# Performance work log

Hardware: AMD Instinct MI355X
Metric: run time of the kernel (lower is better)

Reference implementation:

```python
import math
import jax, jax.numpy as jnp
import numpy as np

EMBED = 512
HEADS = 8
EPS = 1e-5


def _ln(x, gamma, beta):
    mu = jnp.mean(x, axis=-1, keepdims=True)
    var = jnp.mean(jnp.square(x - mu), axis=-1, keepdims=True)
    return (x - mu) * jax.lax.rsqrt(var + EPS) * gamma + beta


def setup_inputs() -> dict:
    key = jax.random.key(0)
    ks = jax.random.split(key, 16)
    D = EMBED
    s = 0.02
    inp = {
        "moves_embeddings": jax.random.normal(ks[0], (4, 2048, D), dtype=jnp.float32),
        "wq": jax.random.normal(ks[1], (D, D), dtype=jnp.float32) * s,
        "bq": jnp.zeros((D,), jnp.float32),
        "wk": jax.random.normal(ks[2], (D, D), dtype=jnp.float32) * s,
        "bk": jnp.zeros((D,), jnp.float32),
        "wv": jax.random.normal(ks[3], (D, D), dtype=jnp.float32) * s,
        "bv": jnp.zeros((D,), jnp.float32),
        "wo": jax.random.normal(ks[4], (D, D), dtype=jnp.float32) * s,
        "bo": jnp.zeros((D,), jnp.float32),
        "w_up": jax.random.normal(ks[5], (D, 4 * D), dtype=jnp.float32) * s,
        "b_up": jnp.zeros((4 * D,), jnp.float32),
        "w_down": jax.random.normal(ks[6], (4 * D, D), dtype=jnp.float32) * s,
        "b_down": jnp.zeros((D,), jnp.float32),
        "g1": jnp.ones((D,), jnp.float32),
        "beta1": jnp.zeros((D,), jnp.float32),
        "g2": jnp.ones((D,), jnp.float32),
        "beta2": jnp.zeros((D,), jnp.float32),
    }
    return inp


def reference(moves_embeddings, wq, bq, wk, bk, wv, bv, wo, bo,
              w_up, b_up, w_down, b_down, g1, beta1, g2, beta2):
    x = moves_embeddings  # [B, S, D]
    B, S, D = x.shape
    Hd = D // HEADS
    # QKV projections, split heads -> [B, H, S, Hd]
    q = (x @ wq + bq).reshape(B, S, HEADS, Hd).transpose(0, 2, 1, 3)
    k = (x @ wk + bk).reshape(B, S, HEADS, Hd).transpose(0, 2, 1, 3)
    v = (x @ wv + bv).reshape(B, S, HEADS, Hd).transpose(0, 2, 1, 3)
    # NOTE: original scales by sqrt(embedding_dim), not sqrt(head_dim)
    scores = jnp.einsum('bhqd,bhkd->bhqk', q, k) / math.sqrt(D)
    attn = jax.nn.softmax(scores, axis=-1)
    ctx = jnp.einsum('bhqk,bhkd->bhqd', attn, v)
    ctx = ctx.transpose(0, 2, 1, 3).reshape(B, S, D)
    y = ctx @ wo + bo
    x = _ln(x + y, g1, beta1)
    # FFN with exact (erf) GELU, matching torch nn.GELU default
    h = jax.nn.gelu(x @ w_up + b_up, approximate=False)
    y = h @ w_down + b_down
    return _ln(x + y, g2, beta2)
```

## Files before the change

### kernel.cpp

```cpp
#include <hip/hip_runtime.h>
#include <math.h>

#define D 512
#define NHEADS 8
#define HD 64
#define SEQ 2048
#define BATCH 4
#define MROWS (BATCH*SEQ)
#define QKVSTR 1536
#define ATT_QSCALE 0.06376228841159383f

typedef short bf16x8 __attribute__((ext_vector_type(8)));
typedef float f32x4 __attribute__((ext_vector_type(4)));
typedef float f32x16 __attribute__((ext_vector_type(16)));

__device__ __forceinline__ ushort f2bf(float f) {
    union { float f; unsigned u; } v; v.f = f;
    unsigned r = (v.u + 0x7fffu + ((v.u >> 16) & 1u)) >> 16;
    return (ushort)r;
}
__device__ __forceinline__ float bf2f(ushort u) {
    union { unsigned u; float f; } v; v.u = ((unsigned)u) << 16; return v.f;
}

__device__ __forceinline__ unsigned cvt_pk_bf16(float lo, float hi_) {
    unsigned r;
    asm("v_cvt_pk_bf16_f32 %0, %1, %2" : "=v"(r) : "v"(lo), "v"(hi_));
    return r;
}

__device__ __forceinline__ float exp2_hw(float x) {
    float r;
    asm("v_exp_f32 %0, %1" : "=v"(r) : "v"(x));
    return r;
}

__device__ __forceinline__ void plswap(unsigned &a, unsigned &b) {
    asm("v_permlane32_swap_b32 %0, %1" : "+v"(a), "+v"(b));
}
__device__ __forceinline__ void plswapf(float &a, float &b) {
    union { float f; unsigned u; } ua, ub;
    ua.f = a; ub.f = b;
    asm("v_permlane32_swap_b32 %0, %1" : "+v"(ua.u), "+v"(ub.u));
    a = ua.f; b = ub.f;
}

__device__ __forceinline__ void gload16(const void* g, void* lds) {
    __builtin_amdgcn_global_load_lds(
        (const __attribute__((address_space(1))) unsigned int*)(uintptr_t)g,
        (__attribute__((address_space(3))) unsigned int*)(uintptr_t)lds,
        16, 0, 0);
}

template<int GELU, int OBF16, int SPLITK>
__global__ __launch_bounds__(512)
void gemm_mfma8(const ushort* __restrict__ A, const ushort* __restrict__ Bt,
                const float* __restrict__ bias, void* __restrict__ Cp,
                void* __restrict__ Cp2, int M, int N, int K)
{
    __shared__ ushort As[2][128 * 64];
    __shared__ ushort Bs[2][128 * 64];

    const int tid = threadIdx.x;
    const int w = tid >> 6, lane = tid & 63;
    const int lr = lane & 15, lg = lane >> 4;
    const int wr = w >> 2, wc = w & 3;
    const int row0 = blockIdx.y * 128, col0 = blockIdx.x * 128;
    const int kLen = SPLITK ? (K >> 1) : K;
    const int kOff = SPLITK ? blockIdx.z * kLen : 0;

    const int srow = lane >> 3;
    const int schunk = (lane & 7) ^ srow;

    const ushort* aSrc = A  + (size_t)(row0 + w * 16 + srow) * K + kOff + schunk * 8;
    const ushort* bSrc = Bt + (size_t)(col0 + w * 16 + srow) * K + kOff + schunk * 8;

    f32x4 acc[4][2] = {};

    auto STAGE = [&](int buf, int k0) {
        ushort* aD = &As[buf][(w * 16) * 64];
        ushort* bD = &Bs[buf][(w * 16) * 64];
        gload16(aSrc + k0,                 aD);
        gload16(aSrc + (size_t)8 * K + k0, aD + 8 * 64);
        gload16(bSrc + k0,                 bD);
        gload16(bSrc + (size_t)8 * K + k0, bD + 8 * 64);
    };

    auto COMPUTE = [&](int buf) {
        const ushort* AsB = As[buf];
        const ushort* BsB = Bs[buf];
        #pragma unroll
        for (int kc = 0; kc < 2; ++kc) {
            bf16x8 af[4], bfr[2];
            #pragma unroll
            for (int mt = 0; mt < 4; ++mt)
                af[mt] = *(const bf16x8*)&AsB[(wr * 64 + mt * 16 + lr) * 64 +
                                             (((kc * 4 + lg) ^ (lr & 7)) * 8)];
            #pragma unroll
            for (int nt = 0; nt < 2; ++nt)
                bfr[nt] = *(const bf16x8*)&BsB[(wc * 32 + nt * 16 + lr) * 64 +
                                              (((kc * 4 + lg) ^ (lr & 7)) * 8)];
            __builtin_amdgcn_s_setprio(1);
            #pragma unroll
            for (int mt = 0; mt < 4; ++mt)
                #pragma unroll
                for (int nt = 0; nt < 2; ++nt)
                    acc[mt][nt] = __builtin_amdgcn_mfma_f32_16x16x32_bf16(
                        af[mt], bfr[nt], acc[mt][nt], 0, 0, 0);
            __builtin_amdgcn_s_setprio(0);
        }
    };

    const int nk = kLen >> 6;
    STAGE(0, 0);
    __syncthreads();
    for (int t = 0; t < nk; ++t) {
        if (t + 1 < nk) STAGE((t + 1) & 1, (t + 1) << 6);
        COMPUTE(t & 1);
        __syncthreads();
    }

    float* Pp = SPLITK ? (blockIdx.z ? (float*)Cp2 : (float*)Cp) : (float*)Cp;
    #pragma unroll
    for (int nt = 0; nt < 2; ++nt) {
        const int col = col0 + wc * 32 + nt * 16 + lr;
        const float bv = SPLITK ? 0.f : bias[col];
        #pragma unroll
        for (int mt = 0; mt < 4; ++mt) {
            #pragma unroll
            for (int i = 0; i < 4; ++i) {
                float o = acc[mt][nt][i] + bv;
                if (GELU) o = 0.5f * o * (1.0f + erff(o * 0.70710678118654752f));
                const size_t idx = (size_t)(row0 + wr * 64 + mt * 16 + lg * 4 + i) * N + col;
                if (OBF16) ((ushort*)Cp)[idx] = f2bf(o);
                else       Pp[idx] = o;
            }
        }
    }
}

__global__ __launch_bounds__(512)
void gemm_qkv8(const ushort* __restrict__ A, const ushort* __restrict__ Bt,
               const float* __restrict__ bias, ushort* __restrict__ qkv,
               ushort* __restrict__ vt)
{
    __shared__ ushort As[2][128 * 64];
    __shared__ ushort Bs[2][128 * 64];

    const int tid = threadIdx.x;
    const int w = tid >> 6, lane = tid & 63;
    const int lr = lane & 15, lg = lane >> 4;
    const int wr = w >> 2, wc = w & 3;
    const int row0 = blockIdx.y * 128, col0 = blockIdx.x * 128;
    const int K = 512;

    const int srow = lane >> 3;
    const int schunk = (lane & 7) ^ srow;

    const ushort* aSrc = A  + (size_t)(row0 + w * 16 + srow) * K + schunk * 8;
    const ushort* bSrc = Bt + (size_t)(col0 + w * 16 + srow) * K + schunk * 8;

    f32x4 acc[4][2] = {};

    auto STAGE = [&](int buf, int k0) {
        ushort* aD = &As[buf][(w * 16) * 64];
        ushort* bD = &Bs[buf][(w * 16) * 64];
        gload16(aSrc + k0,                 aD);
        gload16(aSrc + (size_t)8 * K + k0, aD + 8 * 64);
        gload16(bSrc + k0,                 bD);
        gload16(bSrc + (size_t)8 * K + k0, bD + 8 * 64);
    };

    auto COMPUTE = [&](int buf) {
        const ushort* AsB = As[buf];
        const ushort* BsB = Bs[buf];
        #pragma unroll
        for (int kc = 0; kc < 2; ++kc) {
            bf16x8 af[4], bfr[2];
            #pragma unroll
            for (int mt = 0; mt < 4; ++mt)
                af[mt] = *(const bf16x8*)&AsB[(wr * 64 + mt * 16 + lr) * 64 +
                                             (((kc * 4 + lg) ^ (lr & 7)) * 8)];
            #pragma unroll
            for (int nt = 0; nt < 2; ++nt)
                bfr[nt] = *(const bf16x8*)&BsB[(wc * 32 + nt * 16 + lr) * 64 +
                                              (((kc * 4 + lg) ^ (lr & 7)) * 8)];
            __builtin_amdgcn_s_setprio(1);
            #pragma unroll
            for (int mt = 0; mt < 4; ++mt)
                #pragma unroll
                for (int nt = 0; nt < 2; ++nt)
                    acc[mt][nt] = __builtin_amdgcn_mfma_f32_16x16x32_bf16(
                        af[mt], bfr[nt], acc[mt][nt], 0, 0, 0);
            __builtin_amdgcn_s_setprio(0);
        }
    };

    STAGE(0, 0);
    __syncthreads();
    for (int t = 0; t < 8; ++t) {
        if (t + 1 < 8) STAGE((t + 1) & 1, (t + 1) << 6);
        COMPUTE(t & 1);
        __syncthreads();
    }

    #pragma unroll
    for (int nt = 0; nt < 2; ++nt) {
        const int col = col0 + wc * 32 + nt * 16 + lr;
        const float bv = bias[col];
        if (col < 1024) {
            const float sc = (col < 512) ? ATT_QSCALE : 1.0f;
            #pragma unroll
            for (int mt = 0; mt < 4; ++mt) {
                #pragma unroll
                for (int i = 0; i < 4; ++i) {
                    const float o = (acc[mt][nt][i] + bv) * sc;
                    qkv[(size_t)(row0 + wr * 64 + mt * 16 + lg * 4 + i) * QKVSTR + col] = f2bf(o);
                }
            }
        } else {
            const int hh = (col - 1024) >> 6, d = (col - 1024) & 63;
            #pragma unroll
            for (int mt = 0; mt < 4; ++mt) {
                const int rowb = row0 + wr * 64 + mt * 16 + lg * 4;
                const int bb = rowb >> 11, ss = rowb & (SEQ - 1);
                ushort4 o4;
                o4.x = f2bf(acc[mt][nt][0] + bv);
                o4.y = f2bf(acc[mt][nt][1] + bv);
                o4.z = f2bf(acc[mt][nt][2] + bv);
                o4.w = f2bf(acc[mt][nt][3] + bv);
                *(ushort4*)&vt[((size_t)(bb * NHEADS + hh) * HD + d) * SEQ + ss] = o4;
            }
        }
    }
}

#define KBLK 64
#define NKT (1024 / KBLK)

__global__ __launch_bounds__(512, 4)
void attn_mfma(const ushort* __restrict__ qkv, const ushort* __restrict__ vt,
               ushort* __restrict__ ctx)
{
    __shared__ __align__(16) ushort smem[2][2][2][64 * 64];

    const int tid = threadIdx.x;
    const int lane = tid & 63;
    const int l32 = lane & 31, hi = lane >> 5;
    const int w = tid >> 6;
    const int qsub = w & 3, half = w >> 2;
    const int qt = blockIdx.x, h = blockIdx.y, b = blockIdx.z;
    const int q0 = qt * 128 + qsub * 32;
    const int kbase = half * 1024;

    const size_t seqbase = (size_t)b * SEQ;
    const ushort* Qp = qkv + (seqbase + q0 + l32) * QKVSTR + h * HD;
    const ushort* Kg = qkv + seqbase * QKVSTR + 512 + h * HD;
    const ushort* Vg = vt + (size_t)(b * NHEADS + h) * HD * SEQ;

    bf16x8 qf[4];
    #pragma unroll
    for (int c = 0; c < 4; ++c) qf[c] = *(const bf16x8*)&Qp[c * 16 + hi * 8];

    const int srow = lane >> 3;
    const int sslot = (lane & 7) ^ srow;
    const ushort* pK = Kg + (size_t)(kbase + qsub * 16 + srow) * QKVSTR + sslot * 8;
    const ushort* pV = Vg + (size_t)(qsub * 16 + srow) * SEQ + kbase + sslot * 8;

    f32x16 o0 = {}, o1 = {};
    float l = 0.f;

    auto STAGE = [&](int buf) {
        ushort* dK = &smem[buf][half][0][(qsub * 16) * 64];
        ushort* dV = &smem[buf][half][1][(qsub * 16) * 64];
        gload16(pK,                      dK);
        gload16(pK + (size_t)8 * QKVSTR, dK + 8 * 64);
        gload16(pV,                      dV);
        gload16(pV + (size_t)8 * SEQ,    dV + 8 * 64);
        pK += (size_t)KBLK * QKVSTR;
        pV += KBLK;
    };

    auto COMPUTE = [&](int buf) {
        const ushort* KsH = &smem[buf][half][0][0];
        const ushort* VsH = &smem[buf][half][1][0];

        f32x16 s0 = {}, s1 = {};
        __builtin_amdgcn_s_setprio(1);
        #pragma unroll
        for (int c = 0; c < 4; ++c) {
            const bf16x8 kf0 = *(const bf16x8*)&KsH[l32 * 64 + (((2 * c + hi) ^ (l32 & 7)) * 8)];
            s0 = __builtin_amdgcn_mfma_f32_32x32x16_bf16(kf0, qf[c], s0, 0, 0, 0);
        }
        #pragma unroll
        for (int c = 0; c < 4; ++c) {
            const bf16x8 kf1 = *(const bf16x8*)&KsH[(32 + l32) * 64 + (((2 * c + hi) ^ (l32 & 7)) * 8)];
            s1 = __builtin_amdgcn_mfma_f32_32x32x16_bf16(kf1, qf[c], s1, 0, 0, 0);
        }
        __builtin_amdgcn_s_setprio(0);

        float ts = 0.f;
        #pragma unroll
        for (int r = 0; r < 16; ++r) {
            s0[r] = exp2_hw(s0[r]); ts += s0[r];
            s1[r] = exp2_hw(s1[r]); ts += s1[r];
        }
        l += ts;

        unsigned wp[16];
        #pragma unroll
        for (int j = 0; j < 8; ++j) wp[j]     = cvt_pk_bf16(s0[2 * j], s0[2 * j + 1]);
        #pragma unroll
        for (int j = 0; j < 8; ++j) wp[8 + j] = cvt_pk_bf16(s1[2 * j], s1[2 * j + 1]);
        plswap(wp[0], wp[2]);  plswap(wp[1], wp[3]);
        plswap(wp[4], wp[6]);  plswap(wp[5], wp[7]);
        plswap(wp[8], wp[10]); plswap(wp[9], wp[11]);
        plswap(wp[12], wp[14]); plswap(wp[13], wp[15]);
        union { unsigned u[4]; bf16x8 v; } pb[4];
        #pragma unroll
        for (int kg = 0; kg < 4; ++kg) {
            pb[kg].u[0] = wp[kg * 4 + 0];
            pb[kg].u[1] = wp[kg * 4 + 1];
            pb[kg].u[2] = wp[kg * 4 + 2];
            pb[kg].u[3] = wp[kg * 4 + 3];
        }

        __builtin_amdgcn_s_setprio(1);
        #pragma unroll
        for (int kg = 0; kg < 4; ++kg) {
            const bf16x8 vf0 = *(const bf16x8*)&VsH[l32 * 64 + (((2 * kg + hi) ^ (l32 & 7)) * 8)];
            o0 = __builtin_amdgcn_mfma_f32_32x32x16_bf16(vf0, pb[kg].v, o0, 0, 0, 0);
        }
        #pragma unroll
        for (int kg = 0; kg < 4; ++kg) {
            const bf16x8 vf1 = *(const bf16x8*)&VsH[(32 + l32) * 64 + (((2 * kg + hi) ^ (l32 & 7)) * 8)];
            o1 = __builtin_amdgcn_mfma_f32_32x32x16_bf16(vf1, pb[kg].v, o1, 0, 0, 0);
        }
        __builtin_amdgcn_s_setprio(0);
    };

    STAGE(0);
    __syncthreads();
    for (int tt = 0; tt < NKT; tt += 2) {
        if (tt + 1 < NKT) STAGE(1);
        COMPUTE(0);
        __syncthreads();
        if (tt + 2 < NKT) STAGE(0);
        COMPUTE(1);
        __syncthreads();
    }

    { float a_ = l, b_ = l; plswapf(a_, b_); l = a_ + b_; }

    float* so = (float*)smem;
    float* sl = (float*)((char*)smem + 4 * 64 * 33 * 4);
    if (half) {
        float* row = so + (qsub * 64 + lane) * 33;
        #pragma unroll
        for (int r = 0; r < 16; ++r) row[r] = o0[r];
        #pragma unroll
        for (int r = 0; r < 16; ++r) row[16 + r] = o1[r];
        sl[qsub * 64 + lane] = l;
    }
    __syncthreads();
    if (!half) {
        const float lb = sl[qsub * 64 + lane];
        const float* row = so + (qsub * 64 + lane) * 33;
        const float inv = 1.f / (l + lb);

        ushort* dst = ctx + (seqbase + q0 + l32) * D + h * HD;
        #pragma unroll
        for (int g = 0; g < 4; ++g) {
            ushort4 t0, t1;
            t0.x = f2bf((o0[g * 4 + 0] + row[g * 4 + 0]) * inv);
            t0.y = f2bf((o0[g * 4 + 1] + row[g * 4 + 1]) * inv);
            t0.z = f2bf((o0[g * 4 + 2] + row[g * 4 + 2]) * inv);
            t0.w = f2bf((o0[g * 4 + 3] + row[g * 4 + 3]) * inv);
            t1.x = f2bf((o1[g * 4 + 0] + row[16 + g * 4 + 0]) * inv);
            t1.y = f2bf((o1[g * 4 + 1] + row[16 + g * 4 + 1]) * inv);
            t1.z = f2bf((o1[g * 4 + 2] + row[16 + g * 4 + 2]) * inv);
            t1.w = f2bf((o1[g * 4 + 3] + row[16 + g * 4 + 3]) * inv);
            *(ushort4*)&dst[g * 8 + hi * 4]      = t0;
            *(ushort4*)&dst[32 + g * 8 + hi * 4] = t1;
        }
    }
}

template<int RESBF, int OUTBF>
__global__ __launch_bounds__(256)
void add_ln3(const void* __restrict__ res, const float* __restrict__ b0,
             const float* __restrict__ b1, const float* __restrict__ bias,
             const float* __restrict__ g, const float* __restrict__ beta,
             float* __restrict__ outf, ushort* __restrict__ outb)
{
    const int wave = threadIdx.x >> 6, lane = threadIdx.x & 63;
    const size_t row = (size_t)blockIdx.x * 4 + wave;

    float xr[8];
    if (RESBF) {
        const ushort* pr = (const ushort*)res + row * D + lane * 8;
        const ushort4 r0 = *(const ushort4*)pr;
        const ushort4 r1 = *(const ushort4*)(pr + 4);
        xr[0] = bf2f(r0.x); xr[1] = bf2f(r0.y); xr[2] = bf2f(r0.z); xr[3] = bf2f(r0.w);
        xr[4] = bf2f(r1.x); xr[5] = bf2f(r1.y); xr[6] = bf2f(r1.z); xr[7] = bf2f(r1.w);
    } else {
        const float* pr = (const float*)res + row * D + lane * 8;
        const float4 r0 = *(const float4*)pr;
        const float4 r1 = *(const float4*)(pr + 4);
        xr[0] = r0.x; xr[1] = r0.y; xr[2] = r0.z; xr[3] = r0.w;
        xr[4] = r1.x; xr[5] = r1.y; xr[6] = r1.z; xr[7] = r1.w;
    }

    const float* p0 = &b0[row * D + lane * 8];
    const float* p1 = &b1[row * D + lane * 8];
    const float4 c0 = *(const float4*)p0;
    const float4 c1 = *(const float4*)(p0 + 4);
    const float4 d0 = *(const float4*)p1;
    const float4 d1 = *(const float4*)(p1 + 4);
    const float4 bb0 = *(const float4*)&bias[lane * 8];
    const float4 bb1 = *(const float4*)&bias[lane * 8 + 4];

    float x[8];
    x[0] = xr[0] + c0.x + d0.x + bb0.x; x[1] = xr[1] + c0.y + d0.y + bb0.y;
    x[2] = xr[2] + c0.z + d0.z + bb0.z; x[3] = xr[3] + c0.w + d0.w + bb0.w;
    x[4] = xr[4] + c1.x + d1.x + bb1.x; x[5] = xr[5] + c1.y + d1.y + bb1.y;
    x[6] = xr[6] + c1.z + d1.z + bb1.z; x[7] = xr[7] + c1.w + d1.w + bb1.w;

    float sum = 0.f;
    #pragma unroll
    for (int i = 0; i < 8; ++i) sum += x[i];
    #pragma unroll
    for (int off = 32; off >= 1; off >>= 1) sum += __shfl_xor(sum, off);
    const float mu = sum * (1.0f / D);

    float vsum = 0.f;
    #pragma unroll
    for (int i = 0; i < 8; ++i) { const float dxe = x[i] - mu; vsum += dxe * dxe; }
    #pragma unroll
    for (int off = 32; off >= 1; off >>= 1) vsum += __shfl_xor(vsum, off);
    const float rs = rsqrtf(vsum * (1.0f / D) + 1e-5f);

    const float4 g0  = *(const float4*)&g[lane * 8];
    const float4 g1v = *(const float4*)&g[lane * 8 + 4];
    const float4 be0 = *(const float4*)&beta[lane * 8];
    const float4 be1 = *(const float4*)&beta[lane * 8 + 4];

    float o[8];
    o[0] = (x[0] - mu) * rs * g0.x  + be0.x;
    o[1] = (x[1] - mu) * rs * g0.y  + be0.y;
    o[2] = (x[2] - mu) * rs * g0.z  + be0.z;
    o[3] = (x[3] - mu) * rs * g0.w  + be0.w;
    o[4] = (x[4] - mu) * rs * g1v.x + be1.x;
    o[5] = (x[5] - mu) * rs * g1v.y + be1.y;
    o[6] = (x[6] - mu) * rs * g1v.z + be1.z;
    o[7] = (x[7] - mu) * rs * g1v.w + be1.w;

    if (OUTBF) {
        ushort4 lo, hi;
        lo.x = f2bf(o[0]); lo.y = f2bf(o[1]); lo.z = f2bf(o[2]); lo.w = f2bf(o[3]);
        hi.x = f2bf(o[4]); hi.y = f2bf(o[5]); hi.z = f2bf(o[6]); hi.w = f2bf(o[7]);
        ushort* pq = &outb[row * D + lane * 8];
        *(ushort4*)pq       = lo;
        *(ushort4*)(pq + 4) = hi;
    } else {
        float* po = &outf[row * D + lane * 8];
        *(float4*)po       = *(float4*)&o[0];
        *(float4*)(po + 4) = *(float4*)&o[4];
    }
}

__global__ __launch_bounds__(256)
void prep(const float* __restrict__ x, ushort* __restrict__ x_bf,
          const float* __restrict__ wq, const float* __restrict__ wk,
          const float* __restrict__ wv, const float* __restrict__ wo,
          const float* __restrict__ w_up, const float* __restrict__ w_down,
          ushort* __restrict__ Wt_qkv, ushort* __restrict__ Wt_o,
          ushort* __restrict__ Wt_up, ushort* __restrict__ Wt_down,
          const float* __restrict__ bq, const float* __restrict__ bk,
          const float* __restrict__ bv, float* __restrict__ b_qkv)
{
    const int bid = blockIdx.x;
    const int tid = threadIdx.x;

    if (bid < 2048) {
        const int i = bid * 256 + tid;
        const float4 a = *(const float4*)&x[(size_t)i * 8];
        const float4 b = *(const float4*)&x[(size_t)i * 8 + 4];
        ushort4 lo, hi;
        lo.x = f2bf(a.x); lo.y = f2bf(a.y); lo.z = f2bf(a.z); lo.w = f2bf(a.w);
        hi.x = f2bf(b.x); hi.y = f2bf(b.y); hi.z = f2bf(b.z); hi.w = f2bf(b.w);
        *(ushort4*)&x_bf[(size_t)i * 8]     = lo;
        *(ushort4*)&x_bf[(size_t)i * 8 + 4] = hi;
        return;
    }

    if (bid < 5120) {
        __shared__ float t[32][33];
        const int j = bid - 2048;
        const float* W; ushort* Wt; int N, stride, tI;
        if (j < 256)       { W = wq;     Wt = Wt_qkv;              N = 512;  stride = 512;  tI = j; }
        else if (j < 512)  { W = wk;     Wt = Wt_qkv + 512 * 512;  N = 512;  stride = 512;  tI = j - 256; }
        else if (j < 768)  { W = wv;     Wt = Wt_qkv + 1024 * 512; N = 512;  stride = 512;  tI = j - 512; }
        else if (j < 1024) { W = wo;     Wt = Wt_o;                N = 512;  stride = 512;  tI = j - 768; }
        else if (j < 2048) { W = w_up;   Wt = Wt_up;               N = 2048; stride = 512;  tI = j - 1024; }
        else               { W = w_down; Wt = Wt_down;             N = 512;  stride = 2048; tI = j - 2048; }
        const int ntn = N >> 5;
        const int n0 = (tI % ntn) * 32, k0 = (tI / ntn) * 32;
        const int r = tid >> 5, c = tid & 31;
        #pragma unroll
        for (int i = 0; i < 4; ++i)
            t[r + i * 8][c] = W[(size_t)(k0 + r + i * 8) * N + n0 + c];
        __syncthreads();
        #pragma unroll
        for (int i = 0; i < 4; ++i)
            Wt[(size_t)(n0 + r + i * 8) * stride + k0 + c] = f2bf(t[c][r + i * 8]);
        return;
    }

    const int i = (bid - 5120) * 256 + tid;
    if (i < 1536)
        b_qkv[i] = (i < 512) ? bq[i] : (i < 1024 ? bk[i - 512] : bv[i - 1024]);
}

extern "C" void kernel_launch(void* const* d_in, const int* in_sizes, int n_in,
                              void* d_out, int out_size, void* d_ws, size_t ws_size,
                              hipStream_t stream)
{
    const float* x      = (const float*)d_in[0];
    const float* wq     = (const float*)d_in[1];
    const float* bq     = (const float*)d_in[2];
    const float* wk     = (const float*)d_in[3];
    const float* bk     = (const float*)d_in[4];
    const float* wv     = (const float*)d_in[5];
    const float* bv     = (const float*)d_in[6];
    const float* wo     = (const float*)d_in[7];
    const float* bo     = (const float*)d_in[8];
    const float* w_up   = (const float*)d_in[9];
    const float* b_up   = (const float*)d_in[10];
    const float* w_down = (const float*)d_in[11];
    const float* b_down = (const float*)d_in[12];
    const float* g1     = (const float*)d_in[13];
    const float* beta1  = (const float*)d_in[14];
    const float* g2     = (const float*)d_in[15];
    const float* beta2  = (const float*)d_in[16];
    float* out = (float*)d_out;

    char* wsb = (char*)d_ws;
    #define WS(ofs_mb) (wsb + ((size_t)(ofs_mb) << 20))
    ushort* Wt_qkv  = (ushort*)WS(0);
    ushort* Wt_o    = (ushort*)WS(2);
    ushort* Wt_up   = (ushort*)WS(3);
    ushort* Wt_down = (ushort*)WS(5);
    float*  b_qkv   = (float*) WS(7);
    ushort* x_bf    = (ushort*)WS(8);
    ushort* qkv_bf  = (ushort*)WS(16);
    ushort* vt_bf   = (ushort*)WS(40);
    ushort* ctx_bf  = (ushort*)WS(48);
    float*  yp0     = (float*) WS(8);
    float*  yp1     = (float*) WS(24);
    ushort* x1_bf   = (ushort*)WS(40);
    ushort* h_bf    = (ushort*)WS(8);
    float*  y2p0    = (float*) WS(64);
    float*  y2p1    = (float*) WS(80);
    #undef WS

    const dim3 blk(256), blk8(512);

    prep<<<dim3(5126), blk, 0, stream>>>(x, x_bf, wq, wk, wv, wo, w_up, w_down,
                                         Wt_qkv, Wt_o, Wt_up, Wt_down,
                                         bq, bk, bv, b_qkv);

    gemm_qkv8<<<dim3(12, 64), blk8, 0, stream>>>(x_bf, Wt_qkv, b_qkv, qkv_bf, vt_bf);

    attn_mfma<<<dim3(SEQ / 128, NHEADS, BATCH), blk8, 0, stream>>>(qkv_bf, vt_bf, ctx_bf);

    gemm_mfma8<0, 0, 1><<<dim3(4, 64, 2), blk8, 0, stream>>>(ctx_bf, Wt_o, nullptr, yp0, yp1, MROWS, 512, 512);
    add_ln3<0, 1><<<dim3(MROWS / 4), blk, 0, stream>>>(x, yp0, yp1, bo, g1, beta1, nullptr, x1_bf);

    gemm_mfma8<1, 1, 0><<<dim3(16, 64), blk8, 0, stream>>>(x1_bf, Wt_up, b_up, h_bf, nullptr, MROWS, 2048, 512);
    gemm_mfma8<0, 0, 1><<<dim3(4, 64, 2), blk8, 0, stream>>>(h_bf, Wt_down, nullptr, y2p0, y2p1, MROWS, 512, 2048);
    add_ln3<1, 0><<<dim3(MROWS / 4), blk, 0, stream>>>(x1_bf, y2p0, y2p1, b_down, g2, beta2, out, nullptr);
}
```

Before: 155.3 us.

## Replace GEMM with 256-row tiled, ping-pong pipelined 8-wave MFMA kernel

Replaces the 128x128 double-buffered GEMM with a 256xBN tile kernel that splits the A and B tiles into halves. Global-to-LDS loads of the next k-step are interleaved with four quarter MFMA phases, using explicit vmcnt/lgkmcnt waits and barriers. The larger tiles are meant to raise data reuse per LDS byte and hide load latency for the O-projection, FFN-up and FFN-down GEMMs. In exchange the grid has fewer blocks, register pressure is higher (launch bounds 512,2), and the hand-tuned waitcnt schedule is fragile.

```diff
diff --git a/kernel.cpp b/kernel.cpp
--- a/kernel.cpp
+++ b/kernel.cpp
@@ -52,91 +52,166 @@
         16, 0, 0);
 }
 
-template<int GELU, int OBF16, int SPLITK>
-__global__ __launch_bounds__(512)
-void gemm_mfma8(const ushort* __restrict__ A, const ushort* __restrict__ Bt,
-                const float* __restrict__ bias, void* __restrict__ Cp,
-                void* __restrict__ Cp2, int M, int N, int K)
+template<int BN, int GELU, int OBF16, int SPLITK>
+__global__ __launch_bounds__(512, 2)
+void gemm8p(const ushort* __restrict__ A, const ushort* __restrict__ Bt,
+            const float* __restrict__ bias, void* __restrict__ Cp,
+            void* __restrict__ Cp2, int M, int N, int K)
 {
-    __shared__ ushort As[2][128 * 64];
-    __shared__ ushort Bs[2][128 * 64];
+    constexpr int NR = BN / 64;
+    constexpr int NH = NR / 2;
+    constexpr int BH = BN / 2;
+
+    __shared__ __align__(16) ushort As[2][2][128 * 64];
+    __shared__ __align__(16) ushort Bs[2][2][BH * 64];
 
     const int tid = threadIdx.x;
     const int w = tid >> 6, lane = tid & 63;
     const int lr = lane & 15, lg = lane >> 4;
-    const int wr = w >> 2, wc = w & 3;
-    const int row0 = blockIdx.y * 128, col0 = blockIdx.x * 128;
+    const int wm = w >> 2, wn = w & 3;
+    const int row0 = blockIdx.y * 256, col0 = blockIdx.x * BN;
     const int kLen = SPLITK ? (K >> 1) : K;
     const int kOff = SPLITK ? blockIdx.z * kLen : 0;
+    const int NT = kLen >> 6;
 
     const int srow = lane >> 3;
     const int schunk = (lane & 7) ^ srow;
 
-    const ushort* aSrc = A  + (size_t)(row0 + w * 16 + srow) * K + kOff + schunk * 8;
-    const ushort* bSrc = Bt + (size_t)(col0 + w * 16 + srow) * K + kOff + schunk * 8;
-
-    f32x4 acc[4][2] = {};
-
-    auto STAGE = [&](int buf, int k0) {
-        ushort* aD = &As[buf][(w * 16) * 64];
-        ushort* bD = &Bs[buf][(w * 16) * 64];
-        gload16(aSrc + k0,                 aD);
-        gload16(aSrc + (size_t)8 * K + k0, aD + 8 * 64);
-        gload16(bSrc + k0,                 bD);
-        gload16(bSrc + (size_t)8 * K + k0, bD + 8 * 64);
-    };
-
-    auto COMPUTE = [&](int buf) {
-        const ushort* AsB = As[buf];
-        const ushort* BsB = Bs[buf];
-        #pragma unroll
-        for (int kc = 0; kc < 2; ++kc) {
-            bf16x8 af[4], bfr[2];
-            #pragma unroll
-            for (int mt = 0; mt < 4; ++mt)
-                af[mt] = *(const bf16x8*)&AsB[(wr * 64 + mt * 16 + lr) * 64 +
-                                             (((kc * 4 + lg) ^ (lr & 7)) * 8)];
-            #pragma unroll
-            for (int nt = 0; nt < 2; ++nt)
-                bfr[nt] = *(const bf16x8*)&BsB[(wc * 32 + nt * 16 + lr) * 64 +
-                                              (((kc * 4 + lg) ^ (lr & 7)) * 8)];
-            __builtin_amdgcn_s_setprio(1);
-            #pragma unroll
-            for (int mt = 0; mt < 4; ++mt)
+    const ushort* aS0 = A + (size_t)(row0 + w * 16 + srow) * K + kOff + schunk * 8;
+    const ushort* aS1 = aS0 + (size_t)128 * K;
+    const ushort* bS0;
+    const ushort* bS1;
+    if constexpr (BN == 256) {
+        bS0 = Bt + (size_t)(col0 + w * 16 + srow) * K + kOff + schunk * 8;
+        bS1 = bS0 + (size_t)128 * K;
+    } else {
+        bS0 = Bt + (size_t)(col0 + w * 8 + srow) * K + kOff + schunk * 8;
+        bS1 = bS0 + (size_t)64 * K;
+    }
+
+    auto STA = [&](int b, int h, int t) {
+        const ushort* s = h ? aS1 : aS0;
+        ushort* d = &As[b][h][(w * 16) * 64];
+        gload16(s + t * 64, d);
+        gload16(s + (size_t)8 * K + t * 64, d + 8 * 64);
+    };
+    auto STB = [&](int b, int h, int t) {
+        const ushort* s = h ? bS1 : bS0;
+        if constexpr (BN == 256) {
+            ushort* d = &Bs[b][h][(w * 16) * 64];
+            gload16(s + t * 64, d);
+            gload16(s + (size_t)8 * K + t * 64, d + 8 * 64);
+        } else {
+            ushort* d = &Bs[b][h][(w * 8) * 64];
+            gload16(s + t * 64, d);
+        }
+    };
+
+    const int cW = wn * (BN / 4);
+    const int hB = (cW >= BH) ? 1 : 0;
+    const int rB = cW - hB * BH + lr;
+
+    f32x4 acc[8][NR] = {};
+    bf16x8 bA[4][2], bB[NR][2];
+
+    auto LDA = [&](int b, int mh) {
+        #pragma unroll
+        for (int mt = 0; mt < 4; ++mt)
+            #pragma unroll
+            for (int kk = 0; kk < 2; ++kk)
+                bA[mt][kk] = *(const bf16x8*)&As[b][wm][(mh * 64 + mt * 16 + lr) * 64 +
+                                                       (((kk * 4 + lg) ^ (lr & 7)) * 8)];
+    };
+    auto LDB = [&](int b) {
+        #pragma unroll
+        for (int nt = NR - 1; nt >= 0; --nt)
+            #pragma unroll
+            for (int kk = 0; kk < 2; ++kk)
+                bB[nt][kk] = *(const bf16x8*)&Bs[b][hB][(rB + nt * 16) * 64 +
+                                                       (((kk * 4 + lg) ^ (lr & 7)) * 8)];
+    };
+    auto MFMA = [&](int mh, int nh) {
+        __builtin_amdgcn_s_setprio(1);
+        #pragma unroll
+        for (int mt = 0; mt < 4; ++mt)
+            #pragma unroll
+            for (int j = 0; j < NH; ++j)
                 #pragma unroll
-                for (int nt = 0; nt < 2; ++nt)
-                    acc[mt][nt] = __builtin_amdgcn_mfma_f32_16x16x32_bf16(
-                        af[mt], bfr[nt], acc[mt][nt], 0, 0, 0);
-            __builtin_amdgcn_s_setprio(0);
-        }
-    };
-
-    const int nk = kLen >> 6;
-    STAGE(0, 0);
-    __syncthreads();
-    for (int t = 0; t < nk; ++t) {
-        if (t + 1 < nk) STAGE((t + 1) & 1, (t + 1) << 6);
-        COMPUTE(t & 1);
-        __syncthreads();
-    }
+                for (int kk = 0; kk < 2; ++kk)
+                    acc[mh * 4 + mt][nh * NH + j] = __builtin_amdgcn_mfma_f32_16x16x32_bf16(
+                        bA[mt][kk], bB[nh * NH + j][kk], acc[mh * 4 + mt][nh * NH + j], 0, 0, 0);
+        __builtin_amdgcn_s_setprio(0);
+    };
+    auto VWAIT = [&]() {
+        if constexpr (BN == 256) asm volatile("s_waitcnt vmcnt(6)" ::: "memory");
+        else                     asm volatile("s_waitcnt vmcnt(4)" ::: "memory");
+    };
+    auto LKDRAIN = [&]() {
+        asm volatile("s_waitcnt lgkmcnt(0)" ::: "memory");
+        __builtin_amdgcn_sched_barrier(0);
+    };
+    auto BAR = [&]() { __builtin_amdgcn_s_barrier(); };
+
+    STA(0, 0, 0); STA(0, 1, 0); STB(0, 0, 0); STB(0, 1, 0);
+    STB(1, 0, 1); STB(1, 1, 1); STA(1, 0, 1);
+    VWAIT();
+    BAR();
+
+    for (int T = 0; T + 4 <= NT; T += 2) {
+        LDA(0, 0); LDB(0);
+        STA(1, 1, T + 1);
+        BAR(); MFMA(0, 0); LKDRAIN(); BAR();
+        STB(0, 0, T + 2);
+        BAR(); MFMA(0, 1); BAR();
+        LDA(0, 1);
+        STB(0, 1, T + 2);
+        BAR(); MFMA(1, 0); BAR();
+        STA(0, 0, T + 2);
+        VWAIT();
+        BAR(); MFMA(1, 1); BAR();
+        LDA(1, 0); LDB(1);
+        STA(0, 1, T + 2);
+        BAR(); MFMA(0, 0); LKDRAIN(); BAR();
+        STB(1, 0, T + 3);
+        BAR(); MFMA(0, 1); BAR();
+        LDA(1, 1);
+        STB(1, 1, T + 3);
+        BAR(); MFMA(1, 0); BAR();
+        STA(1, 0, T + 3);
+        VWAIT();
+        BAR(); MFMA(1, 1); BAR();
+    }
+
+    LDA(0, 0); LDB(0);
+    STA(1, 1, NT - 1);
+    MFMA(0, 0); MFMA(0, 1);
+    LDA(0, 1);
+    MFMA(1, 0); MFMA(1, 1);
+    asm volatile("s_waitcnt vmcnt(0)" ::: "memory");
+    BAR();
+    LDA(1, 0); LDB(1);
+    MFMA(0, 0); MFMA(0, 1);
+    LDA(1, 1);
+    MFMA(1, 0); MFMA(1, 1);
 
     float* Pp = SPLITK ? (blockIdx.z ? (float*)Cp2 : (float*)Cp) : (float*)Cp;
     #pragma unroll
-    for (int nt = 0; nt < 2; ++nt) {
-        const int col = col0 + wc * 32 + nt * 16 + lr;
+    for (int nt = 0; nt < NR; ++nt) {
+        const int col = col0 + wn * (BN / 4) + nt * 16 + lr;
         const float bv = SPLITK ? 0.f : bias[col];
         #pragma unroll
-        for (int mt = 0; mt < 4; ++mt) {
+        for (int am = 0; am < 8; ++am) {
             #pragma unroll
             for (int i = 0; i < 4; ++i) {
-                float o = acc[mt][nt][i] + bv;
+                float o = acc[am][nt][i] + bv;
                 if (GELU) o = 0.5f * o * (1.0f + erff(o * 0.70710678118654752f));
-                const size_t idx = (size_t)(row0 + wr * 64 + mt * 16 + lg * 4 + i) * N + col;
+                const size_t idx = (size_t)(row0 + wm * 128 + am * 16 + lg * 4 + i) * N + col;
                 if (OBF16) ((ushort*)Cp)[idx] = f2bf(o);
                 else       Pp[idx] = o;
             }
         }
     }
+    (void)M;
 }
 
 __global__ __launch_bounds__(512)
@@ -574,10 +649,10 @@
 
     attn_mfma<<<dim3(SEQ / 128, NHEADS, BATCH), blk8, 0, stream>>>(qkv_bf, vt_bf, ctx_bf);
 
-    gemm_mfma8<0, 0, 1><<<dim3(4, 64, 2), blk8, 0, stream>>>(ctx_bf, Wt_o, nullptr, yp0, yp1, MROWS, 512, 512);
+    gemm8p<128, 0, 0, 1><<<dim3(4, 32, 2), blk8, 0, stream>>>(ctx_bf, Wt_o, nullptr, yp0, yp1, MROWS, 512, 512);
     add_ln3<0, 1><<<dim3(MROWS / 4), blk, 0, stream>>>(x, yp0, yp1, bo, g1, beta1, nullptr, x1_bf);
 
-    gemm_mfma8<1, 1, 0><<<dim3(16, 64), blk8, 0, stream>>>(x1_bf, Wt_up, b_up, h_bf, nullptr, MROWS, 2048, 512);
-    gemm_mfma8<0, 0, 1><<<dim3(4, 64, 2), blk8, 0, stream>>>(h_bf, Wt_down, nullptr, y2p0, y2p1, MROWS, 512, 2048);
+    gemm8p<256, 1, 1, 0><<<dim3(8, 32), blk8, 0, stream>>>(x1_bf, Wt_up, b_up, h_bf, nullptr, MROWS, 2048, 512);
+    gemm8p<128, 0, 0, 1><<<dim3(4, 32, 2), blk8, 0, stream>>>(h_bf, Wt_down, nullptr, y2p0, y2p1, MROWS, 512, 2048);
     add_ln3<1, 0><<<dim3(MROWS / 4), blk, 0, stream>>>(x1_bf, y2p0, y2p1, b_down, g2, beta2, out, nullptr);
 }
```

Result: slower. 190.6 us (+22.7%).
